# Performance work log

Hardware: AMD Instinct MI355X
Metric: run time of the kernel (lower is better)

## Reference

```python
import jax, jax.numpy as jnp
import numpy as np

B, RATIO, IN_CH, H = 32, 32, 64, 8
E = IN_CH * H                 # embed_dim = in_channels * n_heads = 512
NODES_PER_GRAPH = 512
N = B * NODES_PER_GRAPH       # 16384 source nodes


def setup_inputs() -> dict:
    key = jax.random.key(0)
    ks = jax.random.split(key, 6)
    x = jax.random.normal(ks[0], (N, E), dtype=jnp.float32)
    # edge_index is accepted by forward but unused in 'attn' mode
    edge_index = jax.random.randint(ks[1], (2, 262144), 0, N, dtype=jnp.int32)
    # per-node graph id, sorted, equal-size graphs (batch[-1] + 1 == B)
    batch = jnp.repeat(jnp.arange(B, dtype=jnp.int32), NODES_PER_GRAPH)
    # learned params: cluster query seeds + MultiheadAttention in/out projections
    xcent_base = jax.random.normal(ks[2], (RATIO, E), dtype=jnp.float32)
    in_proj_w = jax.random.normal(ks[3], (3 * E, E), dtype=jnp.float32) / np.sqrt(E).astype(np.float32)
    in_proj_b = jnp.zeros((3 * E,), dtype=jnp.float32)
    out_proj_w = jax.random.normal(ks[4], (E, E), dtype=jnp.float32) / np.sqrt(E).astype(np.float32)
    out_proj_b = jnp.zeros((E,), dtype=jnp.float32)
    return dict(x=x, edge_index=edge_index, batch=batch, xcent_base=xcent_base,
                in_proj_w=in_proj_w, in_proj_b=in_proj_b,
                out_proj_w=out_proj_w, out_proj_b=out_proj_b)


def reference(x, edge_index, batch, xcent_base, in_proj_w, in_proj_b, out_proj_w, out_proj_b):
    # BipartPool.forward, mode='attn':
    #   x_aggrs = xcent_base.repeat(batch_size, 1)  -> queries [L, E], L = B*ratio
    #   MultiheadAttention(q=x_aggrs, k=v=x, attn_mask=mask[batch].T)
    # mask[batch].T is True (disallowed) where query's graph != node's graph.
    L = B * RATIO
    head_dim = E // H
    x_aggrs = jnp.tile(xcent_base, (B, 1))                        # [L, E]

    wq, wk, wv = jnp.split(in_proj_w, 3, axis=0)                  # each [E, E]
    bq, bk, bv = jnp.split(in_proj_b, 3, axis=0)
    q = (x_aggrs @ wq.T + bq).reshape(L, H, head_dim).transpose(1, 0, 2)  # [H, L, hd]
    k = (x @ wk.T + bk).reshape(N, H, head_dim).transpose(1, 0, 2)        # [H, N, hd]
    v = (x @ wv.T + bv).reshape(N, H, head_dim).transpose(1, 0, 2)        # [H, N, hd]

    batchcent = jnp.repeat(jnp.arange(B, dtype=batch.dtype), RATIO)       # [L]
    allowed = batchcent[:, None] == batch[None, :]                        # [L, N]

    scale = np.float32(1.0 / np.sqrt(head_dim))
    scores = jnp.einsum('hld,hnd->hln', q, k) * scale                     # [H, L, N]
    scores = jnp.where(allowed[None], scores, -jnp.inf)
    attn = jax.nn.softmax(scores, axis=-1)
    out = jnp.einsum('hln,hnd->hld', attn, v)                             # [H, L, hd]
    out = out.transpose(1, 0, 2).reshape(L, E)
    xcent = out @ out_proj_w.T + out_proj_b                               # [L, E]
    # original returns (xcent.reshape(B, ratio, E), None, None, batchcent, None, None)
    return xcent.reshape(B, RATIO, E), batchcent
```

## Files before the change

### kernel.cpp

```cpp
#include <hip/hip_runtime.h>
#include <hip/hip_bf16.h>

#define NGRAPH 32
#define NHEAD 8
#define EMB 512
#define NNODES 16384
#define NPG 512
#define LQ 1024
#define PST 520
#define GCH 262144

typedef __attribute__((ext_vector_type(8))) short short8;
typedef __attribute__((ext_vector_type(4))) float f32x4;

static __device__ __forceinline__ unsigned short f2bf(float f) {
  union { float f; unsigned u; } v; v.f = f;
  unsigned r = (v.u + 0x7fffu + ((v.u >> 16) & 1u)) >> 16;
  return (unsigned short)r;
}

static __device__ __forceinline__ short8 cvt8(float4 a, float4 b) {
  short8 r;
  r[0] = f2bf(a.x); r[1] = f2bf(a.y); r[2] = f2bf(a.z); r[3] = f2bf(a.w);
  r[4] = f2bf(b.x); r[5] = f2bf(b.y); r[6] = f2bf(b.z); r[7] = f2bf(b.w);
  return r;
}

static __device__ __forceinline__ void gload_lds16(const ushort* g, ushort* l) {
  __builtin_amdgcn_global_load_lds(
      (const __attribute__((address_space(1))) unsigned*)g,
      (__attribute__((address_space(3))) unsigned*)l, 16, 0, 0);
}

#define BARRIER_LGKM()                                        \
  do {                                                        \
    asm volatile("s_waitcnt lgkmcnt(0)" ::: "memory");        \
    __builtin_amdgcn_s_barrier();                             \
  } while (0)

__global__ __launch_bounds__(256) void prep_all(
    const float* __restrict__ x, const float* __restrict__ wv,
    const float* __restrict__ wo, const float* __restrict__ wq,
    const float* __restrict__ wk, const float* __restrict__ xc,
    const float* __restrict__ bq,
    ushort* __restrict__ xbC, ushort* __restrict__ xbTC,
    ushort* __restrict__ wvb, ushort* __restrict__ wob,
    ushort* __restrict__ PCb, float* __restrict__ bcent) {
  __shared__ ushort smemU[11776];
  const int b = blockIdx.x;
  const int t = threadIdx.x;

  if (b < 32) {
    ushort* Qs  = smemU;
    ushort* WkT = smemU + 2304;
    int h = b >> 2, qs = b & 3;
    int w = t >> 6, lane = t & 63;
    int lr = lane & 15, grp = lane >> 4, ko = grp * 8;

    {
      int dl = t >> 2, cq = t & 3;
      const float* wr = wk + (long)(h * 64 + dl) * EMB + qs * 128;
#pragma unroll
      for (int m = 0; m < 8; ++m) {
        int c0 = cq * 32 + m * 4;
        float4 v = *reinterpret_cast<const float4*>(wr + c0);
        WkT[(c0 + 0) * 72 + dl] = f2bf(0.125f * v.x);
        WkT[(c0 + 1) * 72 + dl] = f2bf(0.125f * v.y);
        WkT[(c0 + 2) * 72 + dl] = f2bf(0.125f * v.z);
        WkT[(c0 + 3) * 72 + dl] = f2bf(0.125f * v.w);
      }
    }

    f32x4 qa[2];
    qa[0] = (f32x4)(0.0f); qa[1] = (f32x4)(0.0f);
#pragma unroll 4
    for (int kk = 0; kk < EMB; kk += 32) {
      const float* xr0 = xc + lr * EMB + kk + ko;
      const float* xr1 = xc + (16 + lr) * EMB + kk + ko;
      const float* wr  = wq + (long)(h * 64 + w * 16 + lr) * EMB + kk + ko;
      short8 a0 = cvt8(*reinterpret_cast<const float4*>(xr0),
                       *reinterpret_cast<const float4*>(xr0 + 4));
      short8 a1 = cvt8(*reinterpret_cast<const float4*>(xr1),
                       *reinterpret_cast<const float4*>(xr1 + 4));
      short8 bb = cvt8(*reinterpret_cast<const float4*>(wr),
                       *reinterpret_cast<const float4*>(wr + 4));
      qa[0] = __builtin_amdgcn_mfma_f32_16x16x32_bf16(a0, bb, qa[0], 0, 0, 0);
      qa[1] = __builtin_amdgcn_mfma_f32_16x16x32_bf16(a1, bb, qa[1], 0, 0, 0);
    }
    float bias = bq[h * 64 + w * 16 + lr];
#pragma unroll
    for (int i = 0; i < 2; ++i)
#pragma unroll
      for (int r = 0; r < 4; ++r)
        Qs[(i * 16 + grp * 4 + r) * 72 + w * 16 + lr] = f2bf(qa[i][r] + bias);
    __syncthreads();

    f32x4 pa[2][2];
#pragma unroll
    for (int i = 0; i < 2; ++i)
#pragma unroll
      for (int j = 0; j < 2; ++j) pa[i][j] = (f32x4)(0.0f);
#pragma unroll
    for (int kk = 0; kk < 64; kk += 32) {
      short8 a0 = *reinterpret_cast<const short8*>(&Qs[lr * 72 + kk + ko]);
      short8 a1 = *reinterpret_cast<const short8*>(&Qs[(16 + lr) * 72 + kk + ko]);
#pragma unroll
      for (int j = 0; j < 2; ++j) {
        short8 bb = *reinterpret_cast<const short8*>(
            &WkT[(w * 32 + j * 16 + lr) * 72 + kk + ko]);
        pa[0][j] = __builtin_amdgcn_mfma_f32_16x16x32_bf16(a0, bb, pa[0][j], 0, 0, 0);
        pa[1][j] = __builtin_amdgcn_mfma_f32_16x16x32_bf16(a1, bb, pa[1][j], 0, 0, 0);
      }
    }
#pragma unroll
    for (int i = 0; i < 2; ++i)
#pragma unroll
      for (int j = 0; j < 2; ++j)
#pragma unroll
        for (int r = 0; r < 4; ++r)
          PCb[(long)(h * 32 + i * 16 + grp * 4 + r) * EMB + qs * 128 + w * 32 + j * 16 + lr] =
              f2bf(pa[i][j][r]);
    return;
  }

  if (b < 544) {
    int off = b - 32;
    const float* src = (off < 256) ? wv : wo;
    ushort* dst = (off < 256) ? wvb : wob;
    off &= 255;
    int i = (off * 256 + t) * 4;
    float4 v = *reinterpret_cast<const float4*>(src + i);
    ushort4 o;
    o.x = f2bf(v.x); o.y = f2bf(v.y); o.z = f2bf(v.z); o.w = f2bf(v.w);
    *reinterpret_cast<ushort4*>(dst + i) = o;
    return;
  }

  if (b == 544) {
#pragma unroll
    for (int p = 0; p < 4; ++p) bcent[t + p * 256] = (float)((t + p * 256) >> 5);
    return;
  }
  if (b < 552) return;

  {
    ushort* tileA = smemU;
    ushort* tileB = smemU + 4608;
    int local = b - 552;
    int xr = local & 7, j = local >> 3;
    int m = j >> 5, r = j & 31;
    int g = xr + 8 * m;
    int bc = r & 7;
    int bl = r >> 3;
    int n0 = bl * 128, e0 = bc * 64;
    int trr = t >> 4, tc = t & 15;

    float4 vA[4], vB[4];
#pragma unroll
    for (int p = 0; p < 4; ++p)
      vA[p] = *reinterpret_cast<const float4*>(
          x + (long)(g * NPG + n0 + trr + p * 16) * EMB + e0 + tc * 4);
#pragma unroll
    for (int p = 0; p < 4; ++p)
      vB[p] = *reinterpret_cast<const float4*>(
          x + (long)(g * NPG + n0 + 64 + trr + p * 16) * EMB + e0 + tc * 4);
#pragma unroll
    for (int p = 0; p < 4; ++p) {
      int n = trr + p * 16;
      ushort4 o;
      o.x = f2bf(vA[p].x); o.y = f2bf(vA[p].y); o.z = f2bf(vA[p].z); o.w = f2bf(vA[p].w);
      *reinterpret_cast<ushort4*>(&tileA[n * 72 + tc * 4]) = o;
    }
#pragma unroll
    for (int p = 0; p < 4; ++p) {
      int n = trr + p * 16;
      ushort4 o;
      o.x = f2bf(vB[p].x); o.y = f2bf(vB[p].y); o.z = f2bf(vB[p].z); o.w = f2bf(vB[p].w);
      *reinterpret_cast<ushort4*>(&tileB[n * 72 + tc * 4]) = o;
    }
    __syncthreads();

    {
      int n = t >> 2, pp = t & 3;
#pragma unroll
      for (int tb = 0; tb < 2; ++tb) {
        const ushort* tile = tb ? tileB : tileA;
        int ng = n0 + tb * 64 + n;
        int sp = pp ^ ((ng >> 1) & 3);
#pragma unroll
        for (int kcq = 0; kcq < 2; ++kcq) {
          int kc = bc * 2 + kcq;
          short8 v = *reinterpret_cast<const short8*>(&tile[n * 72 + kcq * 32 + sp * 8]);
          *reinterpret_cast<short8*>(
              &xbC[(long)g * GCH + kc * 16384 + ng * 32 + pp * 8]) = v;
        }
      }
    }
    {
      int e = t >> 2;
      int eg = e0 + e;
      int sp2 = (t & 3) ^ ((eg >> 1) & 3);
      int rot = t & 7;
#pragma unroll
      for (int tb = 0; tb < 2; ++tb) {
        const ushort* tile = tb ? tileB : tileA;
#pragma unroll
        for (int ncq = 0; ncq < 2; ++ncq) {
          int nc = bl * 4 + tb * 2 + ncq;
          ushort tmp[8];
#pragma unroll
          for (int k = 0; k < 8; ++k) {
            int jj = (k + rot) & 7;
            tmp[jj] = tile[(ncq * 32 + sp2 * 8 + jj) * 72 + e];
          }
          *reinterpret_cast<short8*>(
              &xbTC[(long)g * GCH + nc * 16384 + eg * 32 + (t & 3) * 8]) =
              *reinterpret_cast<short8*>(tmp);
        }
      }
    }
  }
}

__global__ __launch_bounds__(1024) void fused_attn(
    const ushort* __restrict__ PCb, const ushort* __restrict__ xbC,
    const ushort* __restrict__ xbTC, const ushort* __restrict__ wvb,
    const float* __restrict__ bvb, ushort* __restrict__ aout) {
  __shared__ ushort PCl[32 * PST];
  __shared__ ushort PBuf[32 * PST];
  __shared__ ushort Bbuf[2][16384];
  __shared__ float rmax[32][16];
  __shared__ float rsum[32][16];

  const int g = blockIdx.x & 31, h = blockIdx.x >> 5;
  const int t = threadIdx.x, w = t >> 6, lane = t & 63;
  const int lr = lane & 15, grp = lane >> 4;
  const int koU = grp * 8;

  const ushort* xgC  = xbC  + (long)g * GCH;
  const ushort* xgTC = xbTC + (long)g * GCH;

  auto STAGE1 = [&](int c, int db) {
#pragma unroll
    for (int q = 0; q < 2; ++q)
      gload_lds16(xgC + c * 16384 + (w * 32 + q * 16) * 32 + lane * 8,
                  &Bbuf[db][(w * 32 + q * 16) * 32]);
  };
  auto STAGE3 = [&](int c, int db) {
#pragma unroll
    for (int q = 0; q < 2; ++q)
      gload_lds16(xgTC + c * 16384 + (w * 32 + q * 16) * 32 + lane * 8,
                  &Bbuf[db][(w * 32 + q * 16) * 32]);
  };

  STAGE1(0, 0);
  STAGE1(1, 1);
  {
    const ushort* pc = PCb + h * 32 * EMB;
#pragma unroll
    for (int p = 0; p < 2; ++p) {
      int u = t + p * 1024;
      int row = u >> 6, col = (u & 63) * 8;
      *reinterpret_cast<short8*>(&PCl[row * PST + col]) =
          *reinterpret_cast<const short8*>(pc + row * EMB + col);
    }
  }
  BARRIER_LGKM();

  f32x4 acc[2][2];
#pragma unroll
  for (int i = 0; i < 2; ++i)
#pragma unroll
    for (int j = 0; j < 2; ++j) acc[i][j] = (f32x4)(0.0f);

#pragma unroll
  for (int c = 0; c < 16; ++c) {
    const int db = c & 1;
    asm volatile("s_waitcnt vmcnt(2)" ::: "memory");
    __builtin_amdgcn_sched_barrier(0);
    short8 a0 = *reinterpret_cast<const short8*>(&PCl[lr * PST + c * 32 + koU]);
    short8 a1 = *reinterpret_cast<const short8*>(&PCl[(16 + lr) * PST + c * 32 + koU]);
    short8 bv8[2];
#pragma unroll
    for (int j = 0; j < 2; ++j) {
      int n = w * 32 + j * 16 + lr;
      int psrc = grp ^ ((n >> 1) & 3);
      bv8[j] = *reinterpret_cast<const short8*>(&Bbuf[db][n * 32 + psrc * 8]);
    }
#pragma unroll
    for (int j = 0; j < 2; ++j) {
      acc[0][j] = __builtin_amdgcn_mfma_f32_16x16x32_bf16(a0, bv8[j], acc[0][j], 0, 0, 0);
      acc[1][j] = __builtin_amdgcn_mfma_f32_16x16x32_bf16(a1, bv8[j], acc[1][j], 0, 0, 0);
    }
    __builtin_amdgcn_sched_barrier(0);
    if (c < 14) STAGE1(c + 2, db);
    else        STAGE3(c - 14, db);
  }

#pragma unroll
  for (int i = 0; i < 2; ++i)
#pragma unroll
    for (int r = 0; r < 4; ++r) {
      float m = fmaxf(acc[i][0][r], acc[i][1][r]);
      m = fmaxf(m, __shfl_xor(m, 1)); m = fmaxf(m, __shfl_xor(m, 2));
      m = fmaxf(m, __shfl_xor(m, 4)); m = fmaxf(m, __shfl_xor(m, 8));
      if (lr == 0) rmax[i * 16 + grp * 4 + r][w] = m;
    }
  BARRIER_LGKM();
#pragma unroll
  for (int i = 0; i < 2; ++i)
#pragma unroll
    for (int r = 0; r < 4; ++r) {
      int row = i * 16 + grp * 4 + r;
      float m = rmax[row][0];
#pragma unroll
      for (int q = 1; q < 16; ++q) m = fmaxf(m, rmax[row][q]);
      float s = 0.f;
#pragma unroll
      for (int j = 0; j < 2; ++j) {
        float e = __expf(acc[i][j][r] - m);
        acc[i][j][r] = e;
        s += e;
      }
      s += __shfl_xor(s, 1); s += __shfl_xor(s, 2);
      s += __shfl_xor(s, 4); s += __shfl_xor(s, 8);
      if (lr == 0) rsum[row][w] = s;
    }
  BARRIER_LGKM();
#pragma unroll
  for (int i = 0; i < 2; ++i)
#pragma unroll
    for (int r = 0; r < 4; ++r) {
      int row = i * 16 + grp * 4 + r;
      float tot = rsum[row][0];
#pragma unroll
      for (int q = 1; q < 16; ++q) tot += rsum[row][q];
      float inv = 1.f / tot;
#pragma unroll
      for (int j = 0; j < 2; ++j)
        PBuf[row * PST + w * 32 + j * 16 + lr] = f2bf(acc[i][j][r] * inv);
    }
  BARRIER_LGKM();

  f32x4 acc2[2][2];
#pragma unroll
  for (int i = 0; i < 2; ++i)
#pragma unroll
    for (int j = 0; j < 2; ++j) acc2[i][j] = (f32x4)(0.0f);

#pragma unroll
  for (int c = 0; c < 16; ++c) {
    const int db = c & 1;
    if (c < 15) asm volatile("s_waitcnt vmcnt(2)" ::: "memory");
    else        asm volatile("s_waitcnt vmcnt(0)" ::: "memory");
    __builtin_amdgcn_sched_barrier(0);
    short8 a0 = *reinterpret_cast<const short8*>(&PBuf[lr * PST + c * 32 + koU]);
    short8 a1 = *reinterpret_cast<const short8*>(&PBuf[(16 + lr) * PST + c * 32 + koU]);
    short8 bv8[2];
#pragma unroll
    for (int j = 0; j < 2; ++j) {
      int e = w * 32 + j * 16 + lr;
      int psrc = grp ^ ((e >> 1) & 3);
      bv8[j] = *reinterpret_cast<const short8*>(&Bbuf[db][e * 32 + psrc * 8]);
    }
#pragma unroll
    for (int j = 0; j < 2; ++j) {
      acc2[0][j] = __builtin_amdgcn_mfma_f32_16x16x32_bf16(a0, bv8[j], acc2[0][j], 0, 0, 0);
      acc2[1][j] = __builtin_amdgcn_mfma_f32_16x16x32_bf16(a1, bv8[j], acc2[1][j], 0, 0, 0);
    }
    __builtin_amdgcn_sched_barrier(0);
    if (c < 14) STAGE3(c + 2, db);
  }
  BARRIER_LGKM();

#pragma unroll
  for (int i = 0; i < 2; ++i)
#pragma unroll
    for (int r = 0; r < 4; ++r) {
      int row = i * 16 + grp * 4 + r;
#pragma unroll
      for (int j = 0; j < 2; ++j)
        PBuf[row * PST + w * 32 + j * 16 + lr] = f2bf(acc2[i][j][r]);
    }
  BARRIER_LGKM();

  if (w < 8) {
    int wr = w >> 2, wc = w & 3;
    f32x4 acc3 = (f32x4)(0.0f);
    const ushort* wvh = wvb + (long)(h * 64 + wc * 16) * EMB;
#pragma unroll
    for (int c = 0; c < 16; ++c) {
      short8 a = *reinterpret_cast<const short8*>(&PBuf[(wr * 16 + lr) * PST + c * 32 + koU]);
      short8 b = *reinterpret_cast<const short8*>(wvh + (long)lr * EMB + c * 32 + koU);
      acc3 = __builtin_amdgcn_mfma_f32_16x16x32_bf16(a, b, acc3, 0, 0, 0);
    }
    float bias = bvb[h * 64 + wc * 16 + lr];
#pragma unroll
    for (int r = 0; r < 4; ++r) {
      int row = wr * 16 + grp * 4 + r;
      aout[(long)(g * 32 + row) * EMB + h * 64 + wc * 16 + lr] = f2bf(acc3[r] + bias);
    }
  }
}

template <int KK, int FM, int FN, int WM, int WN, bool OUT_BF16, bool HAS_BIAS>
__global__ void gemm_abt(const ushort* __restrict__ A, const ushort* __restrict__ Bm,
                         void* __restrict__ C, const float* __restrict__ bias,
                         int lda, int ldb, int ldc) {
  int tid = threadIdx.x;
  int wave = tid >> 6, lane = tid & 63;
  int wr = wave / WN, wc = wave % WN;
  int rowBase = blockIdx.x * (WM * FM * 16) + wr * FM * 16;
  int colBase = blockIdx.y * (WN * FN * 16) + wc * FN * 16;
  int lr = lane & 15;
  int ko = (lane >> 4) * 8;

  f32x4 acc[FM][FN];
#pragma unroll
  for (int i = 0; i < FM; ++i)
#pragma unroll
    for (int j = 0; j < FN; ++j) acc[i][j] = (f32x4)(0.0f);

#pragma unroll 8
  for (int kk = 0; kk < KK; kk += 32) {
    short8 av[FM], bv[FN];
#pragma unroll
    for (int i = 0; i < FM; ++i)
      av[i] = *reinterpret_cast<const short8*>(A + (long)(rowBase + i * 16 + lr) * lda + kk + ko);
#pragma unroll
    for (int j = 0; j < FN; ++j)
      bv[j] = *reinterpret_cast<const short8*>(Bm + (long)(colBase + j * 16 + lr) * ldb + kk + ko);
#pragma unroll
    for (int i = 0; i < FM; ++i)
#pragma unroll
      for (int j = 0; j < FN; ++j)
        acc[i][j] = __builtin_amdgcn_mfma_f32_16x16x32_bf16(av[i], bv[j], acc[i][j], 0, 0, 0);
  }

  int or0 = (lane >> 4) * 4;
#pragma unroll
  for (int i = 0; i < FM; ++i) {
#pragma unroll
    for (int j = 0; j < FN; ++j) {
      int col = colBase + j * 16 + lr;
      float bval = HAS_BIAS ? bias[col] : 0.f;
#pragma unroll
      for (int r = 0; r < 4; ++r) {
        int row = rowBase + i * 16 + or0 + r;
        float v = acc[i][j][r] + bval;
        if (OUT_BF16)
          ((ushort*)C)[(long)row * ldc + col] = f2bf(v);
        else
          ((float*)C)[(long)row * ldc + col] = v;
      }
    }
  }
}

extern "C" void kernel_launch(void* const* d_in, const int* in_sizes, int n_in,
                              void* d_out, int out_size, void* d_ws, size_t ws_size,
                              hipStream_t stream) {
  const float* x          = (const float*)d_in[0];
  const float* xcent_base = (const float*)d_in[3];
  const float* in_proj_w  = (const float*)d_in[4];
  const float* in_proj_b  = (const float*)d_in[5];
  const float* out_proj_w = (const float*)d_in[6];
  const float* out_proj_b = (const float*)d_in[7];

  char* w = (char*)d_ws;
  ushort* xbC  = (ushort*)(w);
  ushort* xbTC = (ushort*)(w + 16777216);
  ushort* PCb  = (ushort*)(w + 33554432);
  ushort* wvb  = (ushort*)(w + 33816576);
  ushort* wob  = (ushort*)(w + 34340864);
  ushort* aout = (ushort*)(w + 34865152);

  const float* wq = in_proj_w;
  const float* wk = in_proj_w + 512 * 512;
  const float* wv = in_proj_w + 1024 * 512;
  const float* bq = in_proj_b;
  const float* bv = in_proj_b + 1024;

  prep_all<<<1576, 256, 0, stream>>>(x, wv, out_proj_w, wq, wk, xcent_base, bq,
                                     xbC, xbTC, wvb, wob, PCb,
                                     (float*)d_out + (long)LQ * EMB);

  fused_attn<<<256, 1024, 0, stream>>>(PCb, xbC, xbTC, wvb, bv, aout);

  gemm_abt<512, 1, 2, 2, 2, false, true><<<dim3(32, 8, 1), 256, 0, stream>>>(
      aout, wob, d_out, out_proj_b, 512, 512, 512);
}
```

Before: 57.58 us.

## Switch attention score and PV matmuls to FP8 e4m3 MFMA

Converts x, its transposed copy and the projected queries to FP8 e4m3 instead of bf16. Both attention GEMMs (scores and probability-times-x) now use the fp8 MFMA, with rescaling by 1/8 and 64 to keep values in range. This halves the intermediate memory traffic and LDS footprint and relies on higher-throughput fp8 matrix ops. The cost is lower precision: e4m3 quantization of activations and attention probabilities may push accuracy past tolerance.

```diff
diff --git a/kernel.cpp b/kernel.cpp
--- a/kernel.cpp
+++ b/kernel.cpp
@@ -1,5 +1,6 @@
 #include <hip/hip_runtime.h>
 #include <hip/hip_bf16.h>
+#include <hip/hip_fp8.h>
 
 #define NGRAPH 32
 #define NHEAD 8
@@ -7,16 +8,23 @@
 #define NNODES 16384
 #define NPG 512
 #define LQ 1024
-#define PST 520
-#define GCH 262144
+#define PSTB 1040
+#define GCHB 262144
 
 typedef __attribute__((ext_vector_type(8))) short short8;
 typedef __attribute__((ext_vector_type(4))) float f32x4;
+typedef unsigned char u8;
+typedef long long i64;
 
 static __device__ __forceinline__ unsigned short f2bf(float f) {
   union { float f; unsigned u; } v; v.f = f;
   unsigned r = (v.u + 0x7fffu + ((v.u >> 16) & 1u)) >> 16;
   return (unsigned short)r;
+}
+
+static __device__ __forceinline__ u8 f2fp8(float f) {
+  __hip_fp8_e4m3 v(f);
+  return (u8)v.__x;
 }
 
 static __device__ __forceinline__ short8 cvt8(float4 a, float4 b) {
@@ -26,7 +34,12 @@
   return r;
 }
 
-static __device__ __forceinline__ void gload_lds16(const ushort* g, ushort* l) {
+static __device__ __forceinline__ unsigned pk4(float4 v) {
+  return (unsigned)f2fp8(v.x) | ((unsigned)f2fp8(v.y) << 8) |
+         ((unsigned)f2fp8(v.z) << 16) | ((unsigned)f2fp8(v.w) << 24);
+}
+
+static __device__ __forceinline__ void gload_lds16(const u8* g, u8* l) {
   __builtin_amdgcn_global_load_lds(
       (const __attribute__((address_space(1))) unsigned*)g,
       (__attribute__((address_space(3))) unsigned*)l, 16, 0, 0);
@@ -43,10 +56,10 @@
     const float* __restrict__ wo, const float* __restrict__ wq,
     const float* __restrict__ wk, const float* __restrict__ xc,
     const float* __restrict__ bq,
-    ushort* __restrict__ xbC, ushort* __restrict__ xbTC,
+    u8* __restrict__ xbC, u8* __restrict__ xbTC,
     ushort* __restrict__ wvb, ushort* __restrict__ wob,
-    ushort* __restrict__ PCb, float* __restrict__ bcent) {
-  __shared__ ushort smemU[11776];
+    u8* __restrict__ PCb, float* __restrict__ bcent) {
+  __shared__ __align__(16) ushort smemU[11776];
   const int b = blockIdx.x;
   const int t = threadIdx.x;
 
@@ -64,10 +77,10 @@
       for (int m = 0; m < 8; ++m) {
         int c0 = cq * 32 + m * 4;
         float4 v = *reinterpret_cast<const float4*>(wr + c0);
-        WkT[(c0 + 0) * 72 + dl] = f2bf(0.125f * v.x);
-        WkT[(c0 + 1) * 72 + dl] = f2bf(0.125f * v.y);
-        WkT[(c0 + 2) * 72 + dl] = f2bf(0.125f * v.z);
-        WkT[(c0 + 3) * 72 + dl] = f2bf(0.125f * v.w);
+        WkT[(c0 + 0) * 72 + dl] = f2bf(v.x);
+        WkT[(c0 + 1) * 72 + dl] = f2bf(v.y);
+        WkT[(c0 + 2) * 72 + dl] = f2bf(v.z);
+        WkT[(c0 + 3) * 72 + dl] = f2bf(v.w);
       }
     }
 
@@ -118,8 +131,8 @@
       for (int j = 0; j < 2; ++j)
 #pragma unroll
         for (int r = 0; r < 4; ++r)
-          PCb[(long)(h * 32 + i * 16 + grp * 4 + r) * EMB + qs * 128 + w * 32 + j * 16 + lr] =
-              f2bf(pa[i][j][r]);
+          PCb[(long)(h * 32 + i * 16 + grp * 4 + r) * 512 +
+              qs * 128 + w * 32 + j * 16 + lr] = f2fp8(pa[i][j][r]);
     return;
   }
 
@@ -144,8 +157,8 @@
   if (b < 552) return;
 
   {
-    ushort* tileA = smemU;
-    ushort* tileB = smemU + 4608;
+    u8* tileA = (u8*)smemU;
+    u8* tileB = (u8*)smemU + 4608;
     int local = b - 552;
     int xr = local & 7, j = local >> 3;
     int m = j >> 5, r = j & 31;
@@ -165,57 +178,52 @@
       vB[p] = *reinterpret_cast<const float4*>(
           x + (long)(g * NPG + n0 + 64 + trr + p * 16) * EMB + e0 + tc * 4);
 #pragma unroll
-    for (int p = 0; p < 4; ++p) {
-      int n = trr + p * 16;
-      ushort4 o;
-      o.x = f2bf(vA[p].x); o.y = f2bf(vA[p].y); o.z = f2bf(vA[p].z); o.w = f2bf(vA[p].w);
-      *reinterpret_cast<ushort4*>(&tileA[n * 72 + tc * 4]) = o;
-    }
-#pragma unroll
-    for (int p = 0; p < 4; ++p) {
-      int n = trr + p * 16;
-      ushort4 o;
-      o.x = f2bf(vB[p].x); o.y = f2bf(vB[p].y); o.z = f2bf(vB[p].z); o.w = f2bf(vB[p].w);
-      *reinterpret_cast<ushort4*>(&tileB[n * 72 + tc * 4]) = o;
-    }
+    for (int p = 0; p < 4; ++p)
+      *reinterpret_cast<unsigned*>(&tileA[(trr + p * 16) * 72 + tc * 4]) = pk4(vA[p]);
+#pragma unroll
+    for (int p = 0; p < 4; ++p)
+      *reinterpret_cast<unsigned*>(&tileB[(trr + p * 16) * 72 + tc * 4]) = pk4(vB[p]);
     __syncthreads();
 
     {
       int n = t >> 2, pp = t & 3;
 #pragma unroll
       for (int tb = 0; tb < 2; ++tb) {
-        const ushort* tile = tb ? tileB : tileA;
+        const u8* tile = tb ? tileB : tileA;
         int ng = n0 + tb * 64 + n;
         int sp = pp ^ ((ng >> 1) & 3);
 #pragma unroll
         for (int kcq = 0; kcq < 2; ++kcq) {
           int kc = bc * 2 + kcq;
-          short8 v = *reinterpret_cast<const short8*>(&tile[n * 72 + kcq * 32 + sp * 8]);
-          *reinterpret_cast<short8*>(
-              &xbC[(long)g * GCH + kc * 16384 + ng * 32 + pp * 8]) = v;
+          unsigned long long v =
+              *reinterpret_cast<const unsigned long long*>(&tile[n * 72 + kcq * 32 + sp * 8]);
+          *reinterpret_cast<unsigned long long*>(
+              &xbC[(long)g * GCHB + kc * 16384 + ng * 32 + pp * 8]) = v;
         }
       }
     }
     {
       int e = t >> 2;
       int eg = e0 + e;
-      int sp2 = (t & 3) ^ ((eg >> 1) & 3);
-      int rot = t & 7;
+      int pm2 = t & 3;
+      int sp2 = pm2 ^ ((eg >> 1) & 3);
 #pragma unroll
       for (int tb = 0; tb < 2; ++tb) {
-        const ushort* tile = tb ? tileB : tileA;
+        const u8* tile = tb ? tileB : tileA;
 #pragma unroll
         for (int ncq = 0; ncq < 2; ++ncq) {
           int nc = bl * 4 + tb * 2 + ncq;
-          ushort tmp[8];
-#pragma unroll
-          for (int k = 0; k < 8; ++k) {
-            int jj = (k + rot) & 7;
-            tmp[jj] = tile[(ncq * 32 + sp2 * 8 + jj) * 72 + e];
-          }
-          *reinterpret_cast<short8*>(
-              &xbTC[(long)g * GCH + nc * 16384 + eg * 32 + (t & 3) * 8]) =
-              *reinterpret_cast<short8*>(tmp);
+          int base = ncq * 32 + sp2 * 8;
+          unsigned lo = 0, hi = 0;
+#pragma unroll
+          for (int k2 = 0; k2 < 4; ++k2)
+            lo |= (unsigned)tile[(base + k2) * 72 + e] << (8 * k2);
+#pragma unroll
+          for (int k2 = 0; k2 < 4; ++k2)
+            hi |= (unsigned)tile[(base + 4 + k2) * 72 + e] << (8 * k2);
+          long off = (long)g * GCHB + nc * 16384 + eg * 32 + pm2 * 8;
+          *reinterpret_cast<unsigned*>(&xbTC[off]) = lo;
+          *reinterpret_cast<unsigned*>(&xbTC[off + 4]) = hi;
         }
       }
     }
@@ -223,47 +231,35 @@
 }
 
 __global__ __launch_bounds__(1024) void fused_attn(
-    const ushort* __restrict__ PCb, const ushort* __restrict__ xbC,
-    const ushort* __restrict__ xbTC, const ushort* __restrict__ wvb,
+    const u8* __restrict__ PCb, const u8* __restrict__ xbC,
+    const u8* __restrict__ xbTC, const ushort* __restrict__ wvb,
     const float* __restrict__ bvb, ushort* __restrict__ aout) {
-  __shared__ ushort PCl[32 * PST];
-  __shared__ ushort PBuf[32 * PST];
-  __shared__ ushort Bbuf[2][16384];
+  __shared__ __align__(16) u8 PBufB[32 * PSTB];
+  __shared__ __align__(16) u8 BbufB[2][16384];
   __shared__ float rmax[32][16];
   __shared__ float rsum[32][16];
 
   const int g = blockIdx.x & 31, h = blockIdx.x >> 5;
   const int t = threadIdx.x, w = t >> 6, lane = t & 63;
   const int lr = lane & 15, grp = lane >> 4;
-  const int koU = grp * 8;
-
-  const ushort* xgC  = xbC  + (long)g * GCH;
-  const ushort* xgTC = xbTC + (long)g * GCH;
+
+  const u8* xgC  = xbC  + (long)g * GCHB;
+  const u8* xgTC = xbTC + (long)g * GCHB;
 
   auto STAGE1 = [&](int c, int db) {
-#pragma unroll
-    for (int q = 0; q < 2; ++q)
-      gload_lds16(xgC + c * 16384 + (w * 32 + q * 16) * 32 + lane * 8,
-                  &Bbuf[db][(w * 32 + q * 16) * 32]);
+    gload_lds16(xgC + c * 16384 + w * 1024 + lane * 16, &BbufB[db][w * 1024]);
   };
   auto STAGE3 = [&](int c, int db) {
-#pragma unroll
-    for (int q = 0; q < 2; ++q)
-      gload_lds16(xgTC + c * 16384 + (w * 32 + q * 16) * 32 + lane * 8,
-                  &Bbuf[db][(w * 32 + q * 16) * 32]);
+    gload_lds16(xgTC + c * 16384 + w * 1024 + lane * 16, &BbufB[db][w * 1024]);
   };
 
   STAGE1(0, 0);
   STAGE1(1, 1);
   {
-    const ushort* pc = PCb + h * 32 * EMB;
-#pragma unroll
-    for (int p = 0; p < 2; ++p) {
-      int u = t + p * 1024;
-      int row = u >> 6, col = (u & 63) * 8;
-      *reinterpret_cast<short8*>(&PCl[row * PST + col]) =
-          *reinterpret_cast<const short8*>(pc + row * EMB + col);
-    }
+    const u8* pc = PCb + (long)h * 32 * 512;
+    int row = t >> 5, col = (t & 31) * 16;
+    *reinterpret_cast<short8*>(&PBufB[row * PSTB + col]) =
+        *reinterpret_cast<const short8*>(pc + row * 512 + col);
   }
   BARRIER_LGKM();
 
@@ -276,21 +272,21 @@
 #pragma unroll
   for (int c = 0; c < 16; ++c) {
     const int db = c & 1;
-    asm volatile("s_waitcnt vmcnt(2)" ::: "memory");
+    asm volatile("s_waitcnt vmcnt(1)" ::: "memory");
     __builtin_amdgcn_sched_barrier(0);
-    short8 a0 = *reinterpret_cast<const short8*>(&PCl[lr * PST + c * 32 + koU]);
-    short8 a1 = *reinterpret_cast<const short8*>(&PCl[(16 + lr) * PST + c * 32 + koU]);
-    short8 bv8[2];
+    i64 a0 = *reinterpret_cast<const i64*>(&PBufB[lr * PSTB + c * 32 + grp * 8]);
+    i64 a1 = *reinterpret_cast<const i64*>(&PBufB[(16 + lr) * PSTB + c * 32 + grp * 8]);
+    i64 bv8[2];
 #pragma unroll
     for (int j = 0; j < 2; ++j) {
       int n = w * 32 + j * 16 + lr;
       int psrc = grp ^ ((n >> 1) & 3);
-      bv8[j] = *reinterpret_cast<const short8*>(&Bbuf[db][n * 32 + psrc * 8]);
+      bv8[j] = *reinterpret_cast<const i64*>(&BbufB[db][n * 32 + psrc * 8]);
     }
 #pragma unroll
     for (int j = 0; j < 2; ++j) {
-      acc[0][j] = __builtin_amdgcn_mfma_f32_16x16x32_bf16(a0, bv8[j], acc[0][j], 0, 0, 0);
-      acc[1][j] = __builtin_amdgcn_mfma_f32_16x16x32_bf16(a1, bv8[j], acc[1][j], 0, 0, 0);
+      acc[0][j] = __builtin_amdgcn_mfma_f32_16x16x32_fp8_fp8(a0, bv8[j], acc[0][j], 0, 0, 0);
+      acc[1][j] = __builtin_amdgcn_mfma_f32_16x16x32_fp8_fp8(a1, bv8[j], acc[1][j], 0, 0, 0);
     }
     __builtin_amdgcn_sched_barrier(0);
     if (c < 14) STAGE1(c + 2, db);
@@ -301,6 +297,8 @@
   for (int i = 0; i < 2; ++i)
 #pragma unroll
     for (int r = 0; r < 4; ++r) {
+      acc[i][0][r] *= 0.125f;
+      acc[i][1][r] *= 0.125f;
       float m = fmaxf(acc[i][0][r], acc[i][1][r]);
       m = fmaxf(m, __shfl_xor(m, 1)); m = fmaxf(m, __shfl_xor(m, 2));
       m = fmaxf(m, __shfl_xor(m, 4)); m = fmaxf(m, __shfl_xor(m, 8));
@@ -335,10 +333,10 @@
       float tot = rsum[row][0];
 #pragma unroll
       for (int q = 1; q < 16; ++q) tot += rsum[row][q];
-      float inv = 1.f / tot;
+      float inv = 64.f / tot;
 #pragma unroll
       for (int j = 0; j < 2; ++j)
-        PBuf[row * PST + w * 32 + j * 16 + lr] = f2bf(acc[i][j][r] * inv);
+        PBufB[row * PSTB + w * 32 + j * 16 + lr] = f2fp8(acc[i][j][r] * inv);
     }
   BARRIER_LGKM();
 
@@ -351,22 +349,22 @@
 #pragma unroll
   for (int c = 0; c < 16; ++c) {
     const int db = c & 1;
-    if (c < 15) asm volatile("s_waitcnt vmcnt(2)" ::: "memory");
+    if (c < 15) asm volatile("s_waitcnt vmcnt(1)" ::: "memory");
     else        asm volatile("s_waitcnt vmcnt(0)" ::: "memory");
     __builtin_amdgcn_sched_barrier(0);
-    short8 a0 = *reinterpret_cast<const short8*>(&PBuf[lr * PST + c * 32 + koU]);
-    short8 a1 = *reinterpret_cast<const short8*>(&PBuf[(16 + lr) * PST + c * 32 + koU]);
-    short8 bv8[2];
+    i64 a0 = *reinterpret_cast<const i64*>(&PBufB[lr * PSTB + c * 32 + grp * 8]);
+    i64 a1 = *reinterpret_cast<const i64*>(&PBufB[(16 + lr) * PSTB + c * 32 + grp * 8]);
+    i64 bv8[2];
 #pragma unroll
     for (int j = 0; j < 2; ++j) {
       int e = w * 32 + j * 16 + lr;
       int psrc = grp ^ ((e >> 1) & 3);
-      bv8[j] = *reinterpret_cast<const short8*>(&Bbuf[db][e * 32 + psrc * 8]);
+      bv8[j] = *reinterpret_cast<const i64*>(&BbufB[db][e * 32 + psrc * 8]);
     }
 #pragma unroll
     for (int j = 0; j < 2; ++j) {
-      acc2[0][j] = __builtin_amdgcn_mfma_f32_16x16x32_bf16(a0, bv8[j], acc2[0][j], 0, 0, 0);
-      acc2[1][j] = __builtin_amdgcn_mfma_f32_16x16x32_bf16(a1, bv8[j], acc2[1][j], 0, 0, 0);
+      acc2[0][j] = __builtin_amdgcn_mfma_f32_16x16x32_fp8_fp8(a0, bv8[j], acc2[0][j], 0, 0, 0);
+      acc2[1][j] = __builtin_amdgcn_mfma_f32_16x16x32_fp8_fp8(a1, bv8[j], acc2[1][j], 0, 0, 0);
     }
     __builtin_amdgcn_sched_barrier(0);
     if (c < 14) STAGE3(c + 2, db);
@@ -380,19 +378,22 @@
       int row = i * 16 + grp * 4 + r;
 #pragma unroll
       for (int j = 0; j < 2; ++j)
-        PBuf[row * PST + w * 32 + j * 16 + lr] = f2bf(acc2[i][j][r]);
+        *reinterpret_cast<ushort*>(&PBufB[row * PSTB + (w * 32 + j * 16 + lr) * 2]) =
+            f2bf(acc2[i][j][r] * 0.015625f);
     }
   BARRIER_LGKM();
 
   if (w < 8) {
+    const ushort* PBufU = (const ushort*)PBufB;
     int wr = w >> 2, wc = w & 3;
+    int koU = grp * 8;
     f32x4 acc3 = (f32x4)(0.0f);
     const ushort* wvh = wvb + (long)(h * 64 + wc * 16) * EMB;
 #pragma unroll
     for (int c = 0; c < 16; ++c) {
-      short8 a = *reinterpret_cast<const short8*>(&PBuf[(wr * 16 + lr) * PST + c * 32 + koU]);
-      short8 b = *reinterpret_cast<const short8*>(wvh + (long)lr * EMB + c * 32 + koU);
-      acc3 = __builtin_amdgcn_mfma_f32_16x16x32_bf16(a, b, acc3, 0, 0, 0);
+      short8 a = *reinterpret_cast<const short8*>(&PBufU[(wr * 16 + lr) * 520 + c * 32 + koU]);
+      short8 bb = *reinterpret_cast<const short8*>(wvh + (long)lr * EMB + c * 32 + koU);
+      acc3 = __builtin_amdgcn_mfma_f32_16x16x32_bf16(a, bb, acc3, 0, 0, 0);
     }
     float bias = bvb[h * 64 + wc * 16 + lr];
 #pragma unroll
@@ -468,12 +469,12 @@
   const float* out_proj_b = (const float*)d_in[7];
 
   char* w = (char*)d_ws;
-  ushort* xbC  = (ushort*)(w);
-  ushort* xbTC = (ushort*)(w + 16777216);
-  ushort* PCb  = (ushort*)(w + 33554432);
-  ushort* wvb  = (ushort*)(w + 33816576);
-  ushort* wob  = (ushort*)(w + 34340864);
-  ushort* aout = (ushort*)(w + 34865152);
+  u8*     xbC  = (u8*)(w);
+  u8*     xbTC = (u8*)(w + 8388608);
+  u8*     PCb  = (u8*)(w + 16777216);
+  ushort* wvb  = (ushort*)(w + 16908288);
+  ushort* wob  = (ushort*)(w + 17432576);
+  ushort* aout = (ushort*)(w + 17956864);
 
   const float* wq = in_proj_w;
   const float* wk = in_proj_w + 512 * 512;
```

Result: slower. 59.79 us (+3.8%).
